# Kernel tuning notes

Measured on AMD Instinct MI355X. Metric: run time of the kernel, lower is better.

The kernel has to match this reference:

```python
import jax, jax.numpy as jnp
import numpy as np

# Uniform batched-graph layout: B graphs, each with N_PER nodes and E_PER edges.
# Graph g owns nodes [g*N_PER, (g+1)*N_PER) and edges [g*E_PER, (g+1)*E_PER).
B = 256
N_PER = 512
E_PER = 4096
D = 64               # emb_dim
RATIO = 0.25
K = int(RATIO * E_PER)  # edges reserved per graph (causal)


def setup_inputs() -> dict:
    key = jax.random.key(0)
    k_h, k_src, k_dst, k_w1, k_w2 = jax.random.split(key, 5)
    h = jax.random.normal(k_h, (B * N_PER, D), dtype=jnp.float32)
    # edge endpoints local to each graph, then offset into the global node space
    src = jax.random.randint(k_src, (B, E_PER), 0, N_PER, dtype=jnp.int32)
    dst = jax.random.randint(k_dst, (B, E_PER), 0, N_PER, dtype=jnp.int32)
    offs = (jnp.arange(B, dtype=jnp.int32) * N_PER)[:, None]
    edge_index = jnp.stack([(src + offs).reshape(-1), (dst + offs).reshape(-1)])  # [2, B*E_PER]
    batch = jnp.repeat(jnp.arange(B, dtype=jnp.int32), N_PER)  # node -> graph id
    W1 = jax.random.normal(k_w1, (2 * D, 4 * D), dtype=jnp.float32) / np.sqrt(2 * D)
    b1 = jnp.zeros((4 * D,), dtype=jnp.float32)
    W2 = jax.random.normal(k_w2, (4 * D, 1), dtype=jnp.float32) / np.sqrt(4 * D)
    b2 = jnp.zeros((1,), dtype=jnp.float32)
    return {"h": h, "W1": W1, "b1": b1, "W2": W2, "b2": b2,
            "edge_index": edge_index, "batch": batch}


def reference(h, W1, b1, W2, b2, edge_index, batch):
    row, col = edge_index[0], edge_index[1]
    # edge attention MLP: Linear(2D->4D) -> ReLU -> Linear(4D->1)
    edge_rep = jnp.concatenate([h[row], h[col]], axis=-1)          # [E, 2D]
    scores = (jax.nn.relu(edge_rep @ W1 + b1) @ W2 + b2)[:, 0]     # [E] pred_edge_weight

    # segmented top-k per graph (replaces the per-graph CPU argpartition loop)
    s = scores.reshape(B, E_PER)
    order = jnp.argsort(-s, axis=1)                                # descending
    keep = order[:, :K]                                            # causal edge slots
    drop = order[:, K:]                                            # spurious edge slots
    goff = (jnp.arange(B, dtype=keep.dtype) * E_PER)[:, None]
    keep_g = (keep + goff).reshape(-1)                             # [B*K] global edge ids
    drop_g = (drop + goff).reshape(-1)                             # [B*(E_PER-K)]
    causal_edge_weight = scores[keep_g]
    spu_edge_weight = -scores[drop_g]

    # relabel + 'feat' branch with c_pool='add': nodes touched by causal edges,
    # global_add_pool of their embeddings per graph (compaction is index-preserving math)
    ce_row = row[keep_g]
    ce_col = col[keep_g]
    node_mask = jnp.zeros((h.shape[0],), dtype=bool)
    node_mask = node_mask.at[ce_row].set(True).at[ce_col].set(True)
    causal_rep = jax.ops.segment_sum(
        jnp.where(node_mask[:, None], h, jnp.zeros((), h.dtype)),
        batch, num_segments=B)                                     # [B, D]

    return causal_rep, causal_edge_weight, spu_edge_weight
```

## Files before the change

### kernel.cpp

```cpp
#include <hip/hip_runtime.h>
#include <stdint.h>

#define B_GRAPHS 256
#define NPER     512
#define EPER     4096
#define DDIM     64
#define KKEEP    1024
#define HIDDEN   256
#define JT       8
#define NTILE    (HIDDEN/JT)
#define HTILES   (NTILE/2)
#define STR      12

__global__ __launch_bounds__(1024) void scores_kernel(
    const float* __restrict__ h, const float* __restrict__ W1,
    const float* __restrict__ b1, const float* __restrict__ W2,
    const int* __restrict__ edge0, const int* __restrict__ edge1,
    float* __restrict__ sc_part)
{
  __shared__ __align__(16) float At[NPER * STR];
  __shared__ __align__(16) float Bt[NPER * STR];
  const int t  = threadIdx.x;
  const int bid = blockIdx.x;
  const int b  = bid & (B_GRAPHS - 1);
  const int hb = bid >> 8;
  const int half = __builtin_amdgcn_readfirstlane(t >> 9);
  const int n    = t & (NPER - 1);

  float hreg[32];
  const float4* hrow = (const float4*)(h + ((size_t)b * NPER + n) * DDIM + half * 32);
#pragma unroll
  for (int i = 0; i < 8; ++i) {
    float4 v = hrow[i];
    asm volatile("" : "+v"(v.x), "+v"(v.y), "+v"(v.z), "+v"(v.w));
    hreg[4*i+0] = v.x; hreg[4*i+1] = v.y; hreg[4*i+2] = v.z; hreg[4*i+3] = v.w;
  }

  int epk[4];
  float eacc[4];
#pragma unroll
  for (int i = 0; i < 4; ++i) {
    const size_t e = (size_t)b * EPER + t + i * 1024;
    epk[i] = (edge0[e] & (NPER - 1)) | ((edge1[e] & (NPER - 1)) << 16);
    eacc[i] = 0.f;
  }

  const float* __restrict__ W1a = W1 + (size_t)(half * 32) * HIDDEN;
  const float* __restrict__ W1b = W1 + (size_t)(64 + half * 32) * HIDDEN;

  for (int jtt = 0; jtt < HTILES; ++jtt) {
    const int j0 = hb * (HTILES * JT) + jtt * JT;

    float pa[JT], pb[JT];
#pragma unroll
    for (int jj = 0; jj < JT; ++jj) {
      pa[jj] = (half == 0) ? b1[j0 + jj] : 0.f;
      pb[jj] = 0.f;
    }
#pragma unroll
    for (int d = 0; d < 32; ++d) {
      const float hv = hreg[d];
#pragma unroll
      for (int jj = 0; jj < JT; ++jj)
        pa[jj] = fmaf(hv, W1a[d * HIDDEN + j0 + jj], pa[jj]);
#pragma unroll
      for (int jj = 0; jj < JT; ++jj)
        pb[jj] = fmaf(hv, W1b[d * HIDDEN + j0 + jj], pb[jj]);
    }

    if (half) {
      float4 s0 = {pa[0], pa[1], pa[2], pa[3]};
      float4 s1 = {pa[4], pa[5], pa[6], pa[7]};
      ((float4*)(At + n * STR))[0] = s0;
      ((float4*)(At + n * STR))[1] = s1;
    } else {
      float4 s0 = {pb[0], pb[1], pb[2], pb[3]};
      float4 s1 = {pb[4], pb[5], pb[6], pb[7]};
      ((float4*)(Bt + n * STR))[0] = s0;
      ((float4*)(Bt + n * STR))[1] = s1;
    }
    __syncthreads();

    if (half == 0) {
      const float4 o0 = ((const float4*)(At + n * STR))[0];
      const float4 o1 = ((const float4*)(At + n * STR))[1];
      float4 s0 = {pa[0] + o0.x, pa[1] + o0.y, pa[2] + o0.z, pa[3] + o0.w};
      float4 s1 = {pa[4] + o1.x, pa[5] + o1.y, pa[6] + o1.z, pa[7] + o1.w};
      ((float4*)(At + n * STR))[0] = s0;
      ((float4*)(At + n * STR))[1] = s1;
    } else {
      const float4 o0 = ((const float4*)(Bt + n * STR))[0];
      const float4 o1 = ((const float4*)(Bt + n * STR))[1];
      float4 s0 = {pb[0] + o0.x, pb[1] + o0.y, pb[2] + o0.z, pb[3] + o0.w};
      float4 s1 = {pb[4] + o1.x, pb[5] + o1.y, pb[6] + o1.z, pb[7] + o1.w};
      ((float4*)(Bt + n * STR))[0] = s0;
      ((float4*)(Bt + n * STR))[1] = s1;
    }
    __syncthreads();

    float w2r[JT];
#pragma unroll
    for (int jj = 0; jj < JT; ++jj) w2r[jj] = W2[j0 + jj];

#pragma unroll
    for (int i = 0; i < 4; ++i) {
      const int er = epk[i] & 0xffff;
      const int ec = ((unsigned)epk[i]) >> 16;
      const float4* ar = (const float4*)(At + er * STR);
      const float4* br = (const float4*)(Bt + ec * STR);
      const float4 a0 = ar[0], a1 = ar[1];
      const float4 c0 = br[0], c1 = br[1];
      float p = 0.f;
      p = fmaf(fmaxf(a0.x + c0.x, 0.f), w2r[0], p);
      p = fmaf(fmaxf(a0.y + c0.y, 0.f), w2r[1], p);
      p = fmaf(fmaxf(a0.z + c0.z, 0.f), w2r[2], p);
      p = fmaf(fmaxf(a0.w + c0.w, 0.f), w2r[3], p);
      p = fmaf(fmaxf(a1.x + c1.x, 0.f), w2r[4], p);
      p = fmaf(fmaxf(a1.y + c1.y, 0.f), w2r[5], p);
      p = fmaf(fmaxf(a1.z + c1.z, 0.f), w2r[6], p);
      p = fmaf(fmaxf(a1.w + c1.w, 0.f), w2r[7], p);
      eacc[i] += p;
    }
    __syncthreads();
  }

  float* out = sc_part + (size_t)hb * (B_GRAPHS * EPER) + (size_t)b * EPER;
#pragma unroll
  for (int i = 0; i < 4; ++i)
    out[t + i * 1024] = eacc[i];
}

__global__ __launch_bounds__(1024) void sort_kernel(
    const float* __restrict__ scA, const float* __restrict__ scB,
    const float* __restrict__ b2, const int* __restrict__ edge0,
    const int* __restrict__ edge1, const float* __restrict__ h,
    float* __restrict__ out_rep, float* __restrict__ out_cw,
    float* __restrict__ out_sw)
{
  __shared__ unsigned long long keys[EPER];
  __shared__ int mask[NPER];
  __shared__ float red[16 * 64];
  const int t = threadIdx.x;
  const int b = blockIdx.x;
  const float b2v = b2[0];

  if (t < NPER) mask[t] = 0;

#pragma unroll
  for (int i = 0; i < 4; ++i) {
    const int e = t + i * 1024;
    const float s = scA[(size_t)b * EPER + e] + scB[(size_t)b * EPER + e] + b2v;
    unsigned u  = __float_as_uint(s);
    unsigned fk = (u & 0x80000000u) ? ~u : (u | 0x80000000u);
    unsigned dk = ~fk;
    keys[e] = ((unsigned long long)dk << 32) | (unsigned)e;
  }

  for (int k = 2; k <= EPER; k <<= 1) {
    for (int j = k >> 1; j > 0; j >>= 1) {
      __syncthreads();
#pragma unroll
      for (int i = 0; i < 4; ++i) {
        const int p = t + i * 1024;
        const int l = p ^ j;
        if (l > p) {
          const unsigned long long a = keys[p], c = keys[l];
          const bool up = ((p & k) == 0);
          if (up ? (a > c) : (a < c)) { keys[p] = c; keys[l] = a; }
        }
      }
    }
  }
  __syncthreads();

#pragma unroll
  for (int i = 0; i < 4; ++i) {
    const int p = t + i * 1024;
    const unsigned long long key = keys[p];
    const unsigned fk = ~(unsigned)(key >> 32);
    const unsigned u  = (fk & 0x80000000u) ? (fk & 0x7fffffffu) : ~fk;
    const float s = __uint_as_float(u);
    if (p < KKEEP) out_cw[(size_t)b * KKEEP + p] = s;
    else           out_sw[(size_t)b * (EPER - KKEEP) + (p - KKEEP)] = -s;
  }

  {
    const int e = (int)(keys[t] & 0xffffffffu);
    const size_t eg = (size_t)b * EPER + e;
    mask[edge0[eg] & (NPER - 1)] = 1;
    mask[edge1[eg] & (NPER - 1)] = 1;
  }
  __syncthreads();

  {
    const int d = t & 63, g = t >> 6;
    float s = 0.f;
    for (int nn = g; nn < NPER; nn += 16)
      if (mask[nn]) s += h[((size_t)b * NPER + nn) * DDIM + d];
    red[g * 64 + d] = s;
  }
  __syncthreads();
  if (t < 64) {
    float tot = 0.f;
#pragma unroll
    for (int g = 0; g < 16; ++g) tot += red[g * 64 + t];
    out_rep[(size_t)b * DDIM + t] = tot;
  }
}

extern "C" void kernel_launch(void* const* d_in, const int* in_sizes, int n_in,
                              void* d_out, int out_size, void* d_ws, size_t ws_size,
                              hipStream_t stream) {
  const float* h    = (const float*)d_in[0];
  const float* W1   = (const float*)d_in[1];
  const float* b1   = (const float*)d_in[2];
  const float* W2   = (const float*)d_in[3];
  const float* b2   = (const float*)d_in[4];
  const int*   eidx = (const int*)d_in[5];
  const int* edge0 = eidx;
  const int* edge1 = eidx + (size_t)B_GRAPHS * EPER;

  float* sc_part = (float*)d_ws;
  const float* scA = sc_part;
  const float* scB = sc_part + (size_t)B_GRAPHS * EPER;

  float* out     = (float*)d_out;
  float* out_rep = out;
  float* out_cw  = out + B_GRAPHS * DDIM;
  float* out_sw  = out_cw + (size_t)B_GRAPHS * KKEEP;

  scores_kernel<<<B_GRAPHS * 2, 1024, 0, stream>>>(h, W1, b1, W2, edge0, edge1, sc_part);
  sort_kernel<<<B_GRAPHS, 1024, 0, stream>>>(scA, scB, b2, edge0, edge1, h,
                                             out_rep, out_cw, out_sw);
}
```

Baseline: 373.6 us.

## Use one thread per node with full-depth dot product in scores kernel

The scores kernel now uses 512 threads per block, one per node, each computing the full 64-wide projection for both halves instead of splitting the depth across two thread halves. This removes the cross-half reduction through shared memory and one barrier per tile. h is re-read from global/cache on each hidden tile instead of being held in registers, and each thread handles 8 edges instead of 4. Fewer threads per block lowers parallelism within a block while the per-thread FMA work doubles.

```diff
diff --git a/kernel.cpp b/kernel.cpp
--- a/kernel.cpp
+++ b/kernel.cpp
@@ -8,11 +8,10 @@
 #define KKEEP    1024
 #define HIDDEN   256
 #define JT       8
-#define NTILE    (HIDDEN/JT)
-#define HTILES   (NTILE/2)
+#define HTILES   16
 #define STR      12
 
-__global__ __launch_bounds__(1024) void scores_kernel(
+__global__ __launch_bounds__(512) void scores_kernel(
     const float* __restrict__ h, const float* __restrict__ W1,
     const float* __restrict__ b1, const float* __restrict__ W2,
     const int* __restrict__ edge0, const int* __restrict__ edge1,
@@ -20,90 +19,73 @@
 {
   __shared__ __align__(16) float At[NPER * STR];
   __shared__ __align__(16) float Bt[NPER * STR];
-  const int t  = threadIdx.x;
+  const int t   = threadIdx.x;
   const int bid = blockIdx.x;
-  const int b  = bid & (B_GRAPHS - 1);
-  const int hb = bid >> 8;
-  const int half = __builtin_amdgcn_readfirstlane(t >> 9);
-  const int n    = t & (NPER - 1);
-
-  float hreg[32];
-  const float4* hrow = (const float4*)(h + ((size_t)b * NPER + n) * DDIM + half * 32);
+  const int b   = bid & (B_GRAPHS - 1);
+  const int hb  = bid >> 8;
+  const int n   = t;
+
+  int epk[8];
+  float eacc[8];
 #pragma unroll
   for (int i = 0; i < 8; ++i) {
-    float4 v = hrow[i];
-    asm volatile("" : "+v"(v.x), "+v"(v.y), "+v"(v.z), "+v"(v.w));
-    hreg[4*i+0] = v.x; hreg[4*i+1] = v.y; hreg[4*i+2] = v.z; hreg[4*i+3] = v.w;
-  }
-
-  int epk[4];
-  float eacc[4];
-#pragma unroll
-  for (int i = 0; i < 4; ++i) {
-    const size_t e = (size_t)b * EPER + t + i * 1024;
+    const size_t e = (size_t)b * EPER + t + i * 512;
     epk[i] = (edge0[e] & (NPER - 1)) | ((edge1[e] & (NPER - 1)) << 16);
     eacc[i] = 0.f;
   }
 
-  const float* __restrict__ W1a = W1 + (size_t)(half * 32) * HIDDEN;
-  const float* __restrict__ W1b = W1 + (size_t)(64 + half * 32) * HIDDEN;
-
-  for (int jtt = 0; jtt < HTILES; ++jtt) {
-    const int j0 = hb * (HTILES * JT) + jtt * JT;
+  const float* __restrict__ hrow = h + ((size_t)b * NPER + n) * DDIM;
+  const float* __restrict__ W1b_ = W1 + (size_t)DDIM * HIDDEN;
+
+  for (int jt = 0; jt < HTILES; ++jt) {
+    const int j0 = hb * (HTILES * JT) + jt * JT;
+
+    asm volatile("" ::: "memory");
 
     float pa[JT], pb[JT];
 #pragma unroll
-    for (int jj = 0; jj < JT; ++jj) {
-      pa[jj] = (half == 0) ? b1[j0 + jj] : 0.f;
-      pb[jj] = 0.f;
-    }
-#pragma unroll
-    for (int d = 0; d < 32; ++d) {
-      const float hv = hreg[d];
-#pragma unroll
-      for (int jj = 0; jj < JT; ++jj)
-        pa[jj] = fmaf(hv, W1a[d * HIDDEN + j0 + jj], pa[jj]);
-#pragma unroll
-      for (int jj = 0; jj < JT; ++jj)
-        pb[jj] = fmaf(hv, W1b[d * HIDDEN + j0 + jj], pb[jj]);
-    }
-
-    if (half) {
+    for (int jj = 0; jj < JT; ++jj) { pa[jj] = b1[j0 + jj]; pb[jj] = 0.f; }
+
+#pragma unroll
+    for (int dc = 0; dc < 4; ++dc) {
+      const float4* hp = (const float4*)(hrow + dc * 16);
+      float4 h0 = hp[0], h1 = hp[1], h2 = hp[2], h3 = hp[3];
+      float hc[16];
+      hc[0]=h0.x; hc[1]=h0.y; hc[2]=h0.z; hc[3]=h0.w;
+      hc[4]=h1.x; hc[5]=h1.y; hc[6]=h1.z; hc[7]=h1.w;
+      hc[8]=h2.x; hc[9]=h2.y; hc[10]=h2.z; hc[11]=h2.w;
+      hc[12]=h3.x; hc[13]=h3.y; hc[14]=h3.z; hc[15]=h3.w;
+#pragma unroll
+      for (int k = 0; k < 16; ++k) {
+        const int d = dc * 16 + k;
+        const float hv = hc[k];
+#pragma unroll
+        for (int jj = 0; jj < JT; ++jj)
+          pa[jj] = fmaf(hv, W1[d * HIDDEN + j0 + jj], pa[jj]);
+#pragma unroll
+        for (int jj = 0; jj < JT; ++jj)
+          pb[jj] = fmaf(hv, W1b_[d * HIDDEN + j0 + jj], pb[jj]);
+      }
+    }
+
+    {
       float4 s0 = {pa[0], pa[1], pa[2], pa[3]};
       float4 s1 = {pa[4], pa[5], pa[6], pa[7]};
       ((float4*)(At + n * STR))[0] = s0;
       ((float4*)(At + n * STR))[1] = s1;
-    } else {
-      float4 s0 = {pb[0], pb[1], pb[2], pb[3]};
-      float4 s1 = {pb[4], pb[5], pb[6], pb[7]};
-      ((float4*)(Bt + n * STR))[0] = s0;
-      ((float4*)(Bt + n * STR))[1] = s1;
+      float4 u0 = {pb[0], pb[1], pb[2], pb[3]};
+      float4 u1 = {pb[4], pb[5], pb[6], pb[7]};
+      ((float4*)(Bt + n * STR))[0] = u0;
+      ((float4*)(Bt + n * STR))[1] = u1;
     }
     __syncthreads();
 
-    if (half == 0) {
-      const float4 o0 = ((const float4*)(At + n * STR))[0];
-      const float4 o1 = ((const float4*)(At + n * STR))[1];
-      float4 s0 = {pa[0] + o0.x, pa[1] + o0.y, pa[2] + o0.z, pa[3] + o0.w};
-      float4 s1 = {pa[4] + o1.x, pa[5] + o1.y, pa[6] + o1.z, pa[7] + o1.w};
-      ((float4*)(At + n * STR))[0] = s0;
-      ((float4*)(At + n * STR))[1] = s1;
-    } else {
-      const float4 o0 = ((const float4*)(Bt + n * STR))[0];
-      const float4 o1 = ((const float4*)(Bt + n * STR))[1];
-      float4 s0 = {pb[0] + o0.x, pb[1] + o0.y, pb[2] + o0.z, pb[3] + o0.w};
-      float4 s1 = {pb[4] + o1.x, pb[5] + o1.y, pb[6] + o1.z, pb[7] + o1.w};
-      ((float4*)(Bt + n * STR))[0] = s0;
-      ((float4*)(Bt + n * STR))[1] = s1;
-    }
-    __syncthreads();
-
     float w2r[JT];
 #pragma unroll
     for (int jj = 0; jj < JT; ++jj) w2r[jj] = W2[j0 + jj];
 
 #pragma unroll
-    for (int i = 0; i < 4; ++i) {
+    for (int i = 0; i < 8; ++i) {
       const int er = epk[i] & 0xffff;
       const int ec = ((unsigned)epk[i]) >> 16;
       const float4* ar = (const float4*)(At + er * STR);
@@ -126,8 +108,8 @@
 
   float* out = sc_part + (size_t)hb * (B_GRAPHS * EPER) + (size_t)b * EPER;
 #pragma unroll
-  for (int i = 0; i < 4; ++i)
-    out[t + i * 1024] = eacc[i];
+  for (int i = 0; i < 8; ++i)
+    out[t + i * 512] = eacc[i];
 }
 
 __global__ __launch_bounds__(1024) void sort_kernel(
@@ -229,7 +211,7 @@
   float* out_cw  = out + B_GRAPHS * DDIM;
   float* out_sw  = out_cw + (size_t)B_GRAPHS * KKEEP;
 
-  scores_kernel<<<B_GRAPHS * 2, 1024, 0, stream>>>(h, W1, b1, W2, edge0, edge1, sc_part);
+  scores_kernel<<<B_GRAPHS * 2, 512, 0, stream>>>(h, W1, b1, W2, edge0, edge1, sc_part);
   sort_kernel<<<B_GRAPHS, 1024, 0, stream>>>(scA, scB, b2, edge0, edge1, h,
                                              out_rep, out_cw, out_sw);
 }
```

New measurement: 470.9 us. +26.0%, slower.
